# Kernel tuning notes

Hardware: AMD Instinct MI355X
Metric: run time of the kernel (lower is better)

## Reference

```python
import jax, jax.numpy as jnp
import numpy as np

N = 50000      # nodes
E = 800000     # edges (before self-loops)
IN = 256       # in_channels
H = 4          # heads (layer 1)
C = 64         # hidden per head
OUT = 40       # out_channels / classes


def setup_inputs() -> dict:
    key = jax.random.key(0)
    ks = jax.random.split(key, 10)
    s = 0.05  # weight init scale
    return {
        "x": jax.random.normal(ks[0], (N, IN), jnp.float32),
        "edge_index": jax.random.randint(ks[1], (2, E), 0, N),
        "W1": jax.random.normal(ks[2], (IN, H * C), jnp.float32) * s,
        "a_src1": jax.random.normal(ks[3], (H, C), jnp.float32) * s,
        "a_dst1": jax.random.normal(ks[4], (H, C), jnp.float32) * s,
        "b1": jnp.zeros((H * C,), jnp.float32),
        "W2": jax.random.normal(ks[5], (H * C, OUT), jnp.float32) * s,
        "a_src2": jax.random.normal(ks[6], (1, OUT), jnp.float32) * s,
        "a_dst2": jax.random.normal(ks[7], (1, OUT), jnp.float32) * s,
        "b2": jnp.zeros((OUT,), jnp.float32),
    }


def _gat_layer(x, src, dst, W, a_src, a_dst, bias, heads, out_c):
    """PyG GATConv (concat=True, negative_slope=0.2, self-loops already in src/dst)."""
    n = x.shape[0]
    h = (x @ W).reshape(n, heads, out_c)                    # [N,H,C]
    al_s = jnp.sum(h * a_src, axis=-1)                      # [N,H]
    al_d = jnp.sum(h * a_dst, axis=-1)                      # [N,H]
    e = jax.nn.leaky_relu(al_s[src] + al_d[dst], 0.2)       # [Etot,H]
    # edge softmax over incoming edges of each destination node
    m = jax.ops.segment_max(e, dst, num_segments=n)         # [N,H]
    ee = jnp.exp(e - m[dst])
    denom = jax.ops.segment_sum(ee, dst, num_segments=n)
    alpha = ee / (denom[dst] + 1e-16)                       # [Etot,H]
    msg = alpha[:, :, None] * h[src]                        # [Etot,H,C]
    out = jax.ops.segment_sum(msg, dst, num_segments=n)     # [N,H,C]
    return out.reshape(n, heads * out_c) + bias


def reference(x, edge_index, W1, a_src1, a_dst1, b1, W2, a_src2, a_dst2, b2):
    n = x.shape[0]
    loops = jnp.arange(n, dtype=edge_index.dtype)
    src = jnp.concatenate([edge_index[0], loops])
    dst = jnp.concatenate([edge_index[1], loops])
    h = _gat_layer(x, src, dst, W1, a_src1, a_dst1, b1, H, C)   # [N, H*C]
    h = jax.nn.relu(h)
    # F.dropout in eval mode is identity (reference run in eval mode)
    out = _gat_layer(h, src, dst, W2, a_src2, a_dst2, b2, 1, OUT)  # [N, OUT]
    return jax.nn.log_softmax(out, axis=1)
```

## Files before the change

### kernel.cpp

```cpp
#include <hip/hip_runtime.h>
#include <hip/hip_bf16.h>

typedef __hip_bfloat16 bf16;
typedef short v8s __attribute__((ext_vector_type(8)));
typedef float v4f __attribute__((ext_vector_type(4)));

constexpr int NN    = 50000;
constexpr int NE    = 800000;
constexpr int CIN   = 256;
constexpr int HC    = 256;
constexpr int NH    = 4;
constexpr int NOUT  = 40;
constexpr int NPAD  = 48;
constexpr int SCB   = 196;

constexpr size_t al256(size_t x){ return (x + 255) & ~(size_t)255; }
constexpr size_t WS_FLAGS = 0;
constexpr size_t WS_EW1   = 256;
constexpr size_t WS_W1T   = al256(WS_EW1   + (size_t)NE*16);
constexpr size_t WS_AS1N  = al256(WS_W1T   + (size_t)CIN*HC*2);
constexpr size_t WS_AD1N  = al256(WS_AS1N  + HC*2);
constexpr size_t WS_B1N   = al256(WS_AD1N  + HC*2);
constexpr size_t WS_W2T   = al256(WS_B1N   + HC*2);
constexpr size_t WS_AS2N  = al256(WS_W2T   + (size_t)NPAD*HC*2);
constexpr size_t WS_AD2N  = al256(WS_AS2N  + NOUT*2);
constexpr size_t WS_B2N   = al256(WS_AD2N  + NOUT*2);
constexpr size_t WS_COUNTS= al256(WS_B2N   + NOUT*2);
constexpr size_t WS_CURSOR= al256(WS_COUNTS+ (size_t)NN*4);
constexpr size_t WS_ROWPTR= al256(WS_CURSOR+ (size_t)NN*4);
constexpr size_t WS_EIDX  = al256(WS_ROWPTR+ (size_t)(NN+1)*4);
constexpr size_t WS_H1    = al256(WS_EIDX  + (size_t)NE*4);
constexpr size_t WS_ALS1  = al256(WS_H1    + (size_t)NN*HC);
constexpr size_t WS_ALD1  = al256(WS_ALS1  + (size_t)NN*NH*4);
constexpr size_t WS_Y1    = al256(WS_ALD1  + (size_t)NN*NH*4);
constexpr size_t WS_H2    = al256(WS_Y1    + (size_t)NN*HC*2);
constexpr size_t WS_ALS2  = al256(WS_H2    + (size_t)NN*NOUT*2);
constexpr size_t WS_ALD2  = al256(WS_ALS2  + (size_t)NN*4);
constexpr size_t WS_EW2   = al256(WS_ALD2  + (size_t)NN*4);
constexpr size_t WS_BSUM  = al256(WS_EW2   + (size_t)NE*4);
constexpr size_t WS_BOFF  = al256(WS_BSUM  + 1024);

constexpr int CV_W1  = 0;
constexpr int CV_AS1 = CV_W1  + CIN*HC;
constexpr int CV_AD1 = CV_AS1 + HC;
constexpr int CV_B1  = CV_AD1 + HC;
constexpr int CV_W2  = CV_B1  + HC;
constexpr int CV_AS2 = CV_W2  + HC*NOUT;
constexpr int CV_AD2 = CV_AS2 + NOUT;
constexpr int CV_B2  = CV_AD2 + NOUT;
constexpr int CV_HIST= CV_B2  + NOUT;
constexpr int CV_END = CV_HIST + NE;

__device__ __forceinline__ float b2f(bf16 v) { return __bfloat162float(v); }
__device__ __forceinline__ bf16  f2b(float v){ return __float2bfloat16(v); }
__device__ __forceinline__ float bits2f(unsigned short u){ return __uint_as_float(((unsigned)u) << 16); }
__device__ __forceinline__ unsigned short f2bits(float v){
  bf16 t = __float2bfloat16(v);
  return *reinterpret_cast<unsigned short*>(&t);
}
__device__ __forceinline__ float lrelu(float x){ return x > 0.f ? x : 0.2f * x; }

__device__ __forceinline__ float wave_sum(float v){
  #pragma unroll
  for (int off = 32; off; off >>= 1) v += __shfl_xor(v, off, 64);
  return v;
}
__device__ __forceinline__ float wave_max(float v){
  #pragma unroll
  for (int off = 32; off; off >>= 1) v = fmaxf(v, __shfl_xor(v, off, 64));
  return v;
}

__global__ __launch_bounds__(64) void k_detect(const unsigned short* __restrict__ xu,
                                               const unsigned* __restrict__ eu,
                                               int* __restrict__ flags){
  int lane = threadIdx.x;
  int cnt = 0;
  for (int i = lane; i < 256; i += 64){
    int e = (xu[i] >> 7) & 0xFF;
    cnt += (e >= 0x60 && e <= 0x8F) ? 1 : 0;
  }
  #pragma unroll
  for (int off = 32; off; off >>= 1) cnt += __shfl_xor(cnt, off, 64);
  unsigned odd = eu[2 * lane + 1];
  #pragma unroll
  for (int off = 32; off; off >>= 1) odd |= __shfl_xor(odd, off, 64);
  if (lane == 0){
    flags[0] = (cnt < 218) ? 1 : 0;
    flags[1] = (odd == 0)  ? 1 : 0;
  }
}

__device__ __forceinline__ bf16 cvt_b(const void* src, int i, int f32m){
  if (f32m) return __float2bfloat16(((const float*)src)[i]);
  return ((const bf16*)src)[i];
}

__global__ __launch_bounds__(256) void k_convert(
    const void* __restrict__ W1,
    const void* __restrict__ as1,const void* __restrict__ ad1,
    const void* __restrict__ b1, const void* __restrict__ W2,
    const void* __restrict__ as2,const void* __restrict__ ad2,
    const void* __restrict__ b2, const void* __restrict__ ei,
    char* __restrict__ ws){
  const int* flags = (const int*)(ws + WS_FLAGS);
  int f32m = flags[0], i64m = flags[1];
  bf16* w1t  = (bf16*)(ws + WS_W1T);
  bf16* as1n = (bf16*)(ws + WS_AS1N);
  bf16* ad1n = (bf16*)(ws + WS_AD1N);
  bf16* b1n  = (bf16*)(ws + WS_B1N);
  bf16* w2t  = (bf16*)(ws + WS_W2T);
  bf16* as2n = (bf16*)(ws + WS_AS2N);
  bf16* ad2n = (bf16*)(ws + WS_AD2N);
  bf16* b2n  = (bf16*)(ws + WS_B2N);
  int*  counts=(int*) (ws + WS_COUNTS);
  for (int g = blockIdx.x * 256 + threadIdx.x; g < CV_END; g += gridDim.x * 256){
    if      (g < CV_AS1){ int i = g-CV_W1; int k = i >> 8, n = i & 255;
      w1t[n*CIN + k] = cvt_b(W1, i, f32m); }
    else if (g < CV_AD1) as1n[g-CV_AS1] = cvt_b(as1,g-CV_AS1, f32m);
    else if (g < CV_B1 ) ad1n[g-CV_AD1] = cvt_b(ad1,g-CV_AD1, f32m);
    else if (g < CV_W2 ) b1n [g-CV_B1 ] = cvt_b(b1, g-CV_B1,  f32m);
    else if (g < CV_AS2){ int i = g-CV_W2; int k = i / NOUT, n = i - k*NOUT;
      w2t[n*CIN + k] = cvt_b(W2, i, f32m); }
    else if (g < CV_AD2) as2n[g-CV_AS2] = cvt_b(as2,g-CV_AS2, f32m);
    else if (g < CV_B2 ) ad2n[g-CV_AD2] = cvt_b(ad2,g-CV_AD2, f32m);
    else if (g < CV_HIST) b2n[g-CV_B2 ] = cvt_b(b2, g-CV_B2,  f32m);
    else { int i = g-CV_HIST;
      int d = i64m ? (int)((const long long*)ei)[(size_t)NE+i] : ((const int*)ei)[NE+i];
      atomicAdd(&counts[d], 1); }
  }
}

__global__ __launch_bounds__(256) void k_scan_part(const int* __restrict__ counts, int* __restrict__ bsum){
  __shared__ int lds[256];
  int t = threadIdx.x;
  int idx = blockIdx.x * 256 + t;
  int v = (idx < NN) ? counts[idx] : 0;
  lds[t] = v;
  #pragma unroll
  for (int s = 128; s > 0; s >>= 1){
    __syncthreads();
    if (t < s) lds[t] += lds[t + s];
  }
  if (t == 0) bsum[blockIdx.x] = lds[0];
}

__global__ __launch_bounds__(256) void k_scan_mid(const int* __restrict__ bsum, int* __restrict__ boff,
                                                  int* __restrict__ row_ptr){
  __shared__ int lds[256];
  int t = threadIdx.x;
  int v = (t < SCB) ? bsum[t] : 0;
  lds[t] = v;
  for (int off = 1; off < 256; off <<= 1){
    __syncthreads();
    int u = (t >= off) ? lds[t - off] : 0;
    __syncthreads();
    lds[t] += u;
  }
  __syncthreads();
  if (t < SCB) boff[t] = lds[t] - v;
  if (t == 0) row_ptr[NN] = NE;
}

__global__ __launch_bounds__(256) void k_scan_apply(const int* __restrict__ counts, const int* __restrict__ boff,
                                                    int* __restrict__ row_ptr){
  __shared__ int lds[256];
  int t = threadIdx.x;
  int idx = blockIdx.x * 256 + t;
  int v = (idx < NN) ? counts[idx] : 0;
  lds[t] = v;
  for (int off = 1; off < 256; off <<= 1){
    __syncthreads();
    int u = (t >= off) ? lds[t - off] : 0;
    __syncthreads();
    lds[t] += u;
  }
  __syncthreads();
  if (idx < NN) row_ptr[idx] = boff[blockIdx.x] + lds[t] - v;
}

__global__ __launch_bounds__(256) void k_scatter(const void* __restrict__ ei, const int* __restrict__ flags,
                                                 const int* __restrict__ row_ptr,
                                                 int* __restrict__ cursor, int* __restrict__ eidx){
  int i = blockIdx.x * 256 + threadIdx.x;
  if (i >= NE) return;
  int s, d;
  if (flags[1]){ s = (int)((const long long*)ei)[i]; d = (int)((const long long*)ei)[(size_t)NE + i]; }
  else         { s = ((const int*)ei)[i];            d = ((const int*)ei)[NE + i]; }
  int pos = row_ptr[d] + atomicAdd(&cursor[d], 1);
  eidx[pos] = s;
}

constexpr int G1R = 64;
constexpr int LP  = 72;
__global__ __launch_bounds__(256) void k_gemm1(const void* __restrict__ xin,
                                               const int* __restrict__ flags,
                                               const bf16* __restrict__ w1t,
                                               const bf16* __restrict__ as1, const bf16* __restrict__ ad1,
                                               unsigned char* __restrict__ h1q,
                                               float* __restrict__ al_s1, float* __restrict__ al_d1){
  __shared__ short Ab[G1R * LP];
  __shared__ short Bb[256 * LP];
  int tid  = threadIdx.x;
  int w    = tid >> 6, lane = tid & 63, quad = lane >> 4, c = lane & 15;
  int row0 = blockIdx.x * G1R;
  int f32m = flags[0];

  v4f acc[4][4];
  #pragma unroll
  for (int mt = 0; mt < 4; ++mt)
    #pragma unroll
    for (int nt = 0; nt < 4; ++nt) acc[mt][nt] = (v4f){0.f,0.f,0.f,0.f};

  int arow = tid >> 2;
  int aseg = tid & 3;
  int grow = row0 + arow; if (grow >= NN) grow = NN - 1;

  for (int ph = 0; ph < 4; ++ph){
    if (ph) __syncthreads();
    {
      short va[16];
      if (f32m){
        const float* src = (const float*)xin + (size_t)grow * CIN + ph*64 + aseg*16;
        #pragma unroll
        for (int i = 0; i < 4; ++i){
          float4 f = *reinterpret_cast<const float4*>(src + i*4);
          va[i*4+0] = (short)f2bits(f.x); va[i*4+1] = (short)f2bits(f.y);
          va[i*4+2] = (short)f2bits(f.z); va[i*4+3] = (short)f2bits(f.w);
        }
      } else {
        const short* src = (const short*)xin + (size_t)grow * CIN + ph*64 + aseg*16;
        v8s u0 = *reinterpret_cast<const v8s*>(src);
        v8s u1 = *reinterpret_cast<const v8s*>(src + 8);
        #pragma unroll
        for (int i = 0; i < 8; ++i){ va[i] = u0[i]; va[8+i] = u1[i]; }
      }
      short* dst = &Ab[arow * LP + aseg * 16];
      *reinterpret_cast<v8s*>(dst)     = *reinterpret_cast<v8s*>(&va[0]);
      *reinterpret_cast<v8s*>(dst + 8) = *reinterpret_cast<v8s*>(&va[8]);
    }
    {
      const short* src = (const short*)w1t + (size_t)tid * CIN + ph*64;
      short* dst = &Bb[tid * LP];
      #pragma unroll
      for (int j = 0; j < 8; ++j)
        *reinterpret_cast<v8s*>(dst + j*8) = *reinterpret_cast<const v8s*>(src + j*8);
    }
    __syncthreads();
    #pragma unroll
    for (int s = 0; s < 2; ++s){
      int ch = s*4 + quad;
      v8s af[4], bfb[4];
      #pragma unroll
      for (int mt = 0; mt < 4; ++mt)
        af[mt] = *reinterpret_cast<const v8s*>(&Ab[(mt*16 + c) * LP + ch*8]);
      #pragma unroll
      for (int nt = 0; nt < 4; ++nt)
        bfb[nt] = *reinterpret_cast<const v8s*>(&Bb[(w*64 + nt*16 + c) * LP + ch*8]);
      #pragma unroll
      for (int mt = 0; mt < 4; ++mt)
        #pragma unroll
        for (int nt = 0; nt < 4; ++nt)
          acc[mt][nt] = __builtin_amdgcn_mfma_f32_16x16x32_bf16(af[mt], bfb[nt], acc[mt][nt], 0, 0, 0);
    }
  }

  float as1v[4], ad1v[4];
  #pragma unroll
  for (int nt = 0; nt < 4; ++nt){
    as1v[nt] = b2f(as1[w*64 + nt*16 + c]);
    ad1v[nt] = b2f(ad1[w*64 + nt*16 + c]);
  }
  #pragma unroll
  for (int mt = 0; mt < 4; ++mt){
    #pragma unroll
    for (int r = 0; r < 4; ++r){
      float ps = 0.f, pd = 0.f;
      #pragma unroll
      for (int nt = 0; nt < 4; ++nt){ ps += acc[mt][nt][r] * as1v[nt]; pd += acc[mt][nt][r] * ad1v[nt]; }
      #pragma unroll
      for (int off = 1; off < 16; off <<= 1){ ps += __shfl_xor(ps, off, 64); pd += __shfl_xor(pd, off, 64); }
      int row = row0 + mt*16 + quad*4 + r;
      if (c == 0 && row < NN){
        al_s1[row * NH + w] = ps;
        al_d1[row * NH + w] = pd;
      }
    }
  }
  #pragma unroll
  for (int mt = 0; mt < 4; ++mt){
    #pragma unroll
    for (int nt = 0; nt < 4; ++nt){
      #pragma unroll
      for (int r = 0; r < 4; r += 2){
        int row = row0 + mt*16 + quad*4 + r;
        if (row + 1 < NN){
          int pk = __builtin_amdgcn_cvt_pk_fp8_f32(acc[mt][nt][r], acc[mt][nt][r+1], 0, false);
          size_t col = w*64 + nt*16 + c;
          h1q[(size_t)row       * HC + col] = (unsigned char)(pk & 0xFF);
          h1q[(size_t)(row + 1) * HC + col] = (unsigned char)((pk >> 8) & 0xFF);
        } else if (row < NN){
          int pk = __builtin_amdgcn_cvt_pk_fp8_f32(acc[mt][nt][r], acc[mt][nt][r], 0, false);
          h1q[(size_t)row * HC + w*64 + nt*16 + c] = (unsigned char)(pk & 0xFF);
        }
      }
    }
  }
}

__global__ __launch_bounds__(256) void k_ew1(const int* __restrict__ row_ptr, const int* __restrict__ eidx,
                                             const float* __restrict__ al_s1, const float* __restrict__ al_d1,
                                             float4* __restrict__ ew1){
  int lane = threadIdx.x & 63;
  int n = blockIdx.x * 4 + (threadIdx.x >> 6);
  int p0 = __builtin_amdgcn_readfirstlane(row_ptr[n]);
  int p1 = __builtin_amdgcn_readfirstlane(row_ptr[n + 1]);
  float4 ad = reinterpret_cast<const float4*>(al_d1)[n];
  for (int p = p0 + lane; p < p1; p += 64){
    int s = eidx[p];
    float4 as = reinterpret_cast<const float4*>(al_s1)[s];
    float4 w;
    w.x = __expf(lrelu(as.x + ad.x));
    w.y = __expf(lrelu(as.y + ad.y));
    w.z = __expf(lrelu(as.z + ad.z));
    w.w = __expf(lrelu(as.w + ad.w));
    ew1[p] = w;
  }
}

__global__ __launch_bounds__(256) void k_gather1(const int* __restrict__ row_ptr, const int* __restrict__ eidx,
                                                 const float* __restrict__ ew1,
                                                 const float* __restrict__ al_s1, const float* __restrict__ al_d1,
                                                 const unsigned* __restrict__ h1v, const bf16* __restrict__ b1,
                                                 bf16* __restrict__ y1){
  int lane = threadIdx.x & 63;
  int n = blockIdx.x * 4 + (threadIdx.x >> 6);
  int h = lane >> 4;
  int p0 = __builtin_amdgcn_readfirstlane(row_ptr[n]);
  int p1 = __builtin_amdgcn_readfirstlane(row_ptr[n + 1]);
  float wss = __expf(lrelu(al_s1[n * NH + h] + al_d1[n * NH + h]));
  unsigned us = h1v[(size_t)n * 64 + lane];
  float den = wss;
  float a0 = wss * __builtin_amdgcn_cvt_f32_fp8(us, 0);
  float a1 = wss * __builtin_amdgcn_cvt_f32_fp8(us, 1);
  float a2 = wss * __builtin_amdgcn_cvt_f32_fp8(us, 2);
  float a3 = wss * __builtin_amdgcn_cvt_f32_fp8(us, 3);
  int p = p0;
  for (; p + 1 < p1; p += 2){
    int sA = __builtin_amdgcn_readfirstlane(eidx[p]);
    int sB = __builtin_amdgcn_readfirstlane(eidx[p + 1]);
    float wA = ew1[(size_t)p * 4 + h];
    float wB = ew1[(size_t)(p + 1) * 4 + h];
    unsigned uA = h1v[(size_t)sA * 64 + lane];
    unsigned uB = h1v[(size_t)sB * 64 + lane];
    den += wA + wB;
    a0 += wA * __builtin_amdgcn_cvt_f32_fp8(uA, 0) + wB * __builtin_amdgcn_cvt_f32_fp8(uB, 0);
    a1 += wA * __builtin_amdgcn_cvt_f32_fp8(uA, 1) + wB * __builtin_amdgcn_cvt_f32_fp8(uB, 1);
    a2 += wA * __builtin_amdgcn_cvt_f32_fp8(uA, 2) + wB * __builtin_amdgcn_cvt_f32_fp8(uB, 2);
    a3 += wA * __builtin_amdgcn_cvt_f32_fp8(uA, 3) + wB * __builtin_amdgcn_cvt_f32_fp8(uB, 3);
  }
  if (p < p1){
    int s = __builtin_amdgcn_readfirstlane(eidx[p]);
    float w = ew1[(size_t)p * 4 + h];
    unsigned u = h1v[(size_t)s * 64 + lane];
    den += w;
    a0 += w * __builtin_amdgcn_cvt_f32_fp8(u, 0);
    a1 += w * __builtin_amdgcn_cvt_f32_fp8(u, 1);
    a2 += w * __builtin_amdgcn_cvt_f32_fp8(u, 2);
    a3 += w * __builtin_amdgcn_cvt_f32_fp8(u, 3);
  }
  float inv = 1.f / (den + 1e-16f);
  ushort4 bb = reinterpret_cast<const ushort4*>(b1)[lane];
  ushort4 o;
  o.x = f2bits(fmaxf(a0 * inv + bits2f(bb.x), 0.f));
  o.y = f2bits(fmaxf(a1 * inv + bits2f(bb.y), 0.f));
  o.z = f2bits(fmaxf(a2 * inv + bits2f(bb.z), 0.f));
  o.w = f2bits(fmaxf(a3 * inv + bits2f(bb.w), 0.f));
  reinterpret_cast<ushort4*>(y1)[(size_t)n * 64 + lane] = o;
}

constexpr int W2LP = 260;
__global__ __launch_bounds__(256) void k_gemm2(const bf16* __restrict__ y1, const bf16* __restrict__ w2t,
                                               const bf16* __restrict__ as2, const bf16* __restrict__ ad2,
                                               bf16* __restrict__ h2, float* __restrict__ al_s2,
                                               float* __restrict__ al_d2){
  __shared__ short Wb[NPAD * W2LP];
  int tid = threadIdx.x;
  int w = tid >> 6, lane = tid & 63, quad = lane >> 4, c = lane & 15;
  int m0 = blockIdx.x * 64 + w * 16;
  for (int idx = tid; idx < NPAD * 32; idx += 256){
    int n = idx >> 5, sg = idx & 31;
    *reinterpret_cast<v8s*>(&Wb[n * W2LP + sg * 8]) =
      *reinterpret_cast<const v8s*>((const short*)w2t + (size_t)n * CIN + sg * 8);
  }
  int arow = m0 + c; if (arow >= NN) arow = NN - 1;
  const short* ar = (const short*)y1 + (size_t)arow * HC + quad * 8;
  v8s a[8];
  #pragma unroll
  for (int i = 0; i < 8; ++i) a[i] = *reinterpret_cast<const v8s*>(ar + i * 32);
  __syncthreads();

  v4f acc[3];
  #pragma unroll
  for (int t = 0; t < 3; ++t) acc[t] = (v4f){0.f, 0.f, 0.f, 0.f};
  #pragma unroll
  for (int k = 0; k < 8; ++k){
    int ch = k*4 + quad;
    #pragma unroll
    for (int t = 0; t < 3; ++t){
      v8s b = *reinterpret_cast<const v8s*>(&Wb[(t*16 + c) * W2LP + ch * 8]);
      acc[t] = __builtin_amdgcn_mfma_f32_16x16x32_bf16(a[k], b, acc[t], 0, 0, 0);
    }
  }
  float as2f[3], ad2f[3];
  #pragma unroll
  for (int t = 0; t < 3; ++t){
    int col = t*16 + c;
    as2f[t] = (col < NOUT) ? b2f(as2[col]) : 0.f;
    ad2f[t] = (col < NOUT) ? b2f(ad2[col]) : 0.f;
  }
  #pragma unroll
  for (int r = 0; r < 4; ++r){
    int row = m0 + quad*4 + r;
    float ps = 0.f, pd = 0.f;
    #pragma unroll
    for (int t = 0; t < 3; ++t){ ps += acc[t][r] * as2f[t]; pd += acc[t][r] * ad2f[t]; }
    #pragma unroll
    for (int off = 1; off < 16; off <<= 1){ ps += __shfl_xor(ps, off, 64); pd += __shfl_xor(pd, off, 64); }
    if (row < NN){
      if (c == 0){ al_s2[row] = ps; al_d2[row] = pd; }
      #pragma unroll
      for (int t = 0; t < 3; ++t){
        int col = t*16 + c;
        if (col < NOUT) h2[(size_t)row * NOUT + col] = f2b(acc[t][r]);
      }
    }
  }
}

__global__ __launch_bounds__(256) void k_ew2(const int* __restrict__ row_ptr, const int* __restrict__ eidx,
                                             const float* __restrict__ al_s2, const float* __restrict__ al_d2,
                                             float* __restrict__ ew2){
  int lane = threadIdx.x & 63;
  int n = blockIdx.x * 4 + (threadIdx.x >> 6);
  int p0 = __builtin_amdgcn_readfirstlane(row_ptr[n]);
  int p1 = __builtin_amdgcn_readfirstlane(row_ptr[n + 1]);
  float ad = al_d2[n];
  for (int p = p0 + lane; p < p1; p += 64)
    ew2[p] = __expf(lrelu(al_s2[eidx[p]] + ad));
}

__global__ __launch_bounds__(256) void k_gather2(const int* __restrict__ row_ptr, const int* __restrict__ eidx,
                                                 const float* __restrict__ ew2,
                                                 const float* __restrict__ al_s2, const float* __restrict__ al_d2,
                                                 const bf16* __restrict__ h2, const bf16* __restrict__ b2v,
                                                 const int* __restrict__ flags, void* __restrict__ out){
  int lane = threadIdx.x & 63;
  int n = blockIdx.x * 4 + (threadIdx.x >> 6);
  int p0 = __builtin_amdgcn_readfirstlane(row_ptr[n]);
  int p1 = __builtin_amdgcn_readfirstlane(row_ptr[n + 1]);
  float wss = __expf(lrelu(al_s2[n] + al_d2[n]));
  float den = wss;
  float acc = (lane < NOUT) ? wss * b2f(h2[(size_t)n * NOUT + lane]) : 0.f;
  int p = p0;
  for (; p + 1 < p1; p += 2){
    int sA = __builtin_amdgcn_readfirstlane(eidx[p]);
    int sB = __builtin_amdgcn_readfirstlane(eidx[p + 1]);
    float wA = ew2[p], wB = ew2[p + 1];
    float hA = 0.f, hB = 0.f;
    if (lane < NOUT){
      hA = b2f(h2[(size_t)sA * NOUT + lane]);
      hB = b2f(h2[(size_t)sB * NOUT + lane]);
    }
    den += wA + wB;
    acc += wA * hA + wB * hB;
  }
  if (p < p1){
    int s = __builtin_amdgcn_readfirstlane(eidx[p]);
    float w = ew2[p];
    den += w;
    if (lane < NOUT) acc += w * b2f(h2[(size_t)s * NOUT + lane]);
  }
  float v = (lane < NOUT) ? (acc / (den + 1e-16f) + b2f(b2v[lane])) : -INFINITY;
  float M = wave_max(v);
  float ex = (lane < NOUT) ? __expf(v - M) : 0.f;
  float S = wave_sum(ex);
  if (lane < NOUT){
    float r = v - M - __logf(S);
    size_t idx = (size_t)n * NOUT + lane;
    if (flags[0]) ((float*)out)[idx] = r;
    else          ((bf16*)out)[idx]  = f2b(r);
  }
}

extern "C" void kernel_launch(void* const* d_in, const int* in_sizes, int n_in,
                              void* d_out, int out_size, void* d_ws, size_t ws_size,
                              hipStream_t stream) {
  const void* x   = d_in[0];
  const void* ei  = d_in[1];
  const void* W1  = d_in[2];
  const void* as1 = d_in[3];
  const void* ad1 = d_in[4];
  const void* b1  = d_in[5];
  const void* W2  = d_in[6];
  const void* as2 = d_in[7];
  const void* ad2 = d_in[8];
  const void* b2  = d_in[9];

  char* ws = (char*)d_ws;
  int*   flags   = (int*)  (ws + WS_FLAGS);
  float* ew1     = (float*)(ws + WS_EW1);
  bf16*  w1t     = (bf16*) (ws + WS_W1T);
  bf16*  as1n    = (bf16*) (ws + WS_AS1N);
  bf16*  ad1n    = (bf16*) (ws + WS_AD1N);
  bf16*  b1n     = (bf16*) (ws + WS_B1N);
  bf16*  w2t     = (bf16*) (ws + WS_W2T);
  bf16*  as2n    = (bf16*) (ws + WS_AS2N);
  bf16*  ad2n    = (bf16*) (ws + WS_AD2N);
  bf16*  b2n     = (bf16*) (ws + WS_B2N);
  int*   counts  = (int*)  (ws + WS_COUNTS);
  int*   cursor  = (int*)  (ws + WS_CURSOR);
  int*   row_ptr = (int*)  (ws + WS_ROWPTR);
  int*   eidx    = (int*)  (ws + WS_EIDX);
  unsigned char* h1q = (unsigned char*)(ws + WS_H1);
  float* al_s1   = (float*)(ws + WS_ALS1);
  float* al_d1   = (float*)(ws + WS_ALD1);
  bf16*  y1      = (bf16*) (ws + WS_Y1);
  bf16*  h2      = (bf16*) (ws + WS_H2);
  float* al_s2   = (float*)(ws + WS_ALS2);
  float* al_d2   = (float*)(ws + WS_ALD2);
  float* ew2     = (float*)(ws + WS_EW2);
  int*   bsum    = (int*)  (ws + WS_BSUM);
  int*   boff    = (int*)  (ws + WS_BOFF);

  hipMemsetAsync(counts, 0, (size_t)NN * 4, stream);
  hipMemsetAsync(cursor, 0, (size_t)NN * 4, stream);
  hipMemsetAsync(w2t,    0, (size_t)NPAD * CIN * 2, stream);

  k_detect <<<1, 64, 0, stream>>>((const unsigned short*)x, (const unsigned*)ei, flags);
  k_convert<<<1024, 256, 0, stream>>>(W1, as1, ad1, b1, W2, as2, ad2, b2, ei, ws);

  int eb = (NE + 255) / 256;
  k_scan_part <<<SCB, 256, 0, stream>>>(counts, bsum);
  k_scan_mid  <<<1, 256, 0, stream>>>(bsum, boff, row_ptr);
  k_scan_apply<<<SCB, 256, 0, stream>>>(counts, boff, row_ptr);
  k_scatter<<<eb, 256, 0, stream>>>(ei, flags, row_ptr, cursor, eidx);

  k_gemm1  <<<(NN + G1R - 1) / G1R, 256, 0, stream>>>(x, flags, w1t, as1n, ad1n, h1q, al_s1, al_d1);
  k_ew1    <<<NN / 4, 256, 0, stream>>>(row_ptr, eidx, al_s1, al_d1, (float4*)ew1);
  k_gather1<<<NN / 4, 256, 0, stream>>>(row_ptr, eidx, ew1, al_s1, al_d1, (const unsigned*)h1q, b1n, y1);
  k_gemm2  <<<(NN + 63) / 64, 256, 0, stream>>>(y1, w2t, as2n, ad2n, h2, al_s2, al_d2);
  k_ew2    <<<NN / 4, 256, 0, stream>>>(row_ptr, eidx, al_s2, al_d2, ew2);
  k_gather2<<<NN / 4, 256, 0, stream>>>(row_ptr, eidx, ew2, al_s2, al_d2, h2, b2n, flags, d_out);
}
```

Measured before the change: 342.5 us.

## Replace global-atomic CSR scatter with two-pass bucketed scatter by destination block

The single-pass edge scatter, which did a global atomic per edge on random destination cursors, becomes a two-level bucket sort. Edges are first histogrammed and scattered into 256-node destination buckets using LDS atomics. A per-bucket refine pass then does the final CSR placement with localized global atomics. The aim is better locality for the cursor atomics and the eidx writes, at the cost of three extra launches, a small single-block scan and an intermediate int2 edge buffer.

```diff
diff --git a/kernel.cpp b/kernel.cpp
--- a/kernel.cpp
+++ b/kernel.cpp
@@ -13,6 +13,9 @@
 constexpr int NOUT  = 40;
 constexpr int NPAD  = 48;
 constexpr int SCB   = 196;
+constexpr int B1    = 128;
+constexpr int CH    = (NE + B1 - 1) / B1;
+constexpr int NB    = (NN + 255) >> 8;
 
 constexpr size_t al256(size_t x){ return (x + 255) & ~(size_t)255; }
 constexpr size_t WS_FLAGS = 0;
@@ -39,6 +42,10 @@
 constexpr size_t WS_EW2   = al256(WS_ALD2  + (size_t)NN*4);
 constexpr size_t WS_BSUM  = al256(WS_EW2   + (size_t)NE*4);
 constexpr size_t WS_BOFF  = al256(WS_BSUM  + 1024);
+constexpr size_t WS_GCNT  = al256(WS_BOFF  + 1024);
+constexpr size_t WS_ROFF  = al256(WS_GCNT  + (size_t)256*B1*4);
+constexpr size_t WS_BBASE = al256(WS_ROFF  + (size_t)256*B1*4);
+constexpr size_t WS_EBUF  = al256(WS_BBASE + 1056);
 
 constexpr int CV_W1  = 0;
 constexpr int CV_AS1 = CV_W1  + CIN*HC;
@@ -179,16 +186,73 @@
   if (idx < NN) row_ptr[idx] = boff[blockIdx.x] + lds[t] - v;
 }
 
-__global__ __launch_bounds__(256) void k_scatter(const void* __restrict__ ei, const int* __restrict__ flags,
-                                                 const int* __restrict__ row_ptr,
-                                                 int* __restrict__ cursor, int* __restrict__ eidx){
-  int i = blockIdx.x * 256 + threadIdx.x;
-  if (i >= NE) return;
-  int s, d;
-  if (flags[1]){ s = (int)((const long long*)ei)[i]; d = (int)((const long long*)ei)[(size_t)NE + i]; }
-  else         { s = ((const int*)ei)[i];            d = ((const int*)ei)[NE + i]; }
-  int pos = row_ptr[d] + atomicAdd(&cursor[d], 1);
-  eidx[pos] = s;
+__global__ __launch_bounds__(256) void k_lhist(const void* __restrict__ ei, const int* __restrict__ flags,
+                                               int* __restrict__ gcnt){
+  __shared__ int h[256];
+  int tid = threadIdx.x, blk = blockIdx.x;
+  h[tid] = 0;
+  __syncthreads();
+  int i0 = blk * CH, i1 = min(i0 + CH, NE);
+  int i64m = flags[1];
+  for (int i = i0 + tid; i < i1; i += 256){
+    int d = i64m ? (int)((const long long*)ei)[(size_t)NE + i] : ((const int*)ei)[NE + i];
+    atomicAdd(&h[d >> 8], 1);
+  }
+  __syncthreads();
+  gcnt[tid * B1 + blk] = h[tid];
+}
+
+__global__ __launch_bounds__(256) void k_gscan(const int* __restrict__ gcnt, int* __restrict__ roff,
+                                               int* __restrict__ bbase){
+  __shared__ int lds[256];
+  int t = threadIdx.x;
+  int tot = 0;
+  for (int blk = 0; blk < B1; ++blk) tot += gcnt[t * B1 + blk];
+  lds[t] = tot;
+  for (int off = 1; off < 256; off <<= 1){
+    __syncthreads();
+    int u = (t >= off) ? lds[t - off] : 0;
+    __syncthreads();
+    lds[t] += u;
+  }
+  __syncthreads();
+  int base = lds[t] - tot;
+  bbase[t] = base;
+  if (t == 255) bbase[256] = NE;
+  int run = base;
+  for (int blk = 0; blk < B1; ++blk){
+    roff[t * B1 + blk] = run;
+    run += gcnt[t * B1 + blk];
+  }
+}
+
+__global__ __launch_bounds__(256) void k_bscatter(const void* __restrict__ ei, const int* __restrict__ flags,
+                                                  const int* __restrict__ roff, int2* __restrict__ ebuf){
+  __shared__ int lcur[256];
+  int tid = threadIdx.x, blk = blockIdx.x;
+  lcur[tid] = roff[tid * B1 + blk];
+  __syncthreads();
+  int i0 = blk * CH, i1 = min(i0 + CH, NE);
+  int i64m = flags[1];
+  for (int i = i0 + tid; i < i1; i += 256){
+    int s, d;
+    if (i64m){ s = (int)((const long long*)ei)[i]; d = (int)((const long long*)ei)[(size_t)NE + i]; }
+    else     { s = ((const int*)ei)[i];            d = ((const int*)ei)[NE + i]; }
+    int pos = atomicAdd(&lcur[d >> 8], 1);
+    ebuf[pos] = make_int2(s, d);
+  }
+}
+
+__global__ __launch_bounds__(256) void k_refine(const int2* __restrict__ ebuf, const int* __restrict__ bbase,
+                                                const int* __restrict__ row_ptr, int* __restrict__ cursor,
+                                                int* __restrict__ eidx){
+  int b = blockIdx.x;
+  int p0 = bbase[b], p1 = bbase[b + 1];
+  for (int p = p0 + threadIdx.x; p < p1; p += 256){
+    int2 e = ebuf[p];
+    int pos = row_ptr[e.y] + atomicAdd(&cursor[e.y], 1);
+    eidx[pos] = e.x;
+  }
 }
 
 constexpr int G1R = 64;
@@ -532,6 +596,10 @@
   float* ew2     = (float*)(ws + WS_EW2);
   int*   bsum    = (int*)  (ws + WS_BSUM);
   int*   boff    = (int*)  (ws + WS_BOFF);
+  int*   gcnt    = (int*)  (ws + WS_GCNT);
+  int*   roff    = (int*)  (ws + WS_ROFF);
+  int*   bbase   = (int*)  (ws + WS_BBASE);
+  int2*  ebuf    = (int2*) (ws + WS_EBUF);
 
   hipMemsetAsync(counts, 0, (size_t)NN * 4, stream);
   hipMemsetAsync(cursor, 0, (size_t)NN * 4, stream);
@@ -540,11 +608,13 @@
   k_detect <<<1, 64, 0, stream>>>((const unsigned short*)x, (const unsigned*)ei, flags);
   k_convert<<<1024, 256, 0, stream>>>(W1, as1, ad1, b1, W2, as2, ad2, b2, ei, ws);
 
-  int eb = (NE + 255) / 256;
+  k_lhist   <<<B1, 256, 0, stream>>>(ei, flags, gcnt);
+  k_gscan   <<<1, 256, 0, stream>>>(gcnt, roff, bbase);
   k_scan_part <<<SCB, 256, 0, stream>>>(counts, bsum);
   k_scan_mid  <<<1, 256, 0, stream>>>(bsum, boff, row_ptr);
   k_scan_apply<<<SCB, 256, 0, stream>>>(counts, boff, row_ptr);
-  k_scatter<<<eb, 256, 0, stream>>>(ei, flags, row_ptr, cursor, eidx);
+  k_bscatter<<<B1, 256, 0, stream>>>(ei, flags, roff, ebuf);
+  k_refine  <<<NB, 256, 0, stream>>>(ebuf, bbase, row_ptr, cursor, eidx);
 
   k_gemm1  <<<(NN + G1R - 1) / G1R, 256, 0, stream>>>(x, flags, w1t, as1n, ad1n, h1q, al_s1, al_d1);
   k_ew1    <<<NN / 4, 256, 0, stream>>>(row_ptr, eidx, al_s1, al_d1, (float4*)ew1);
```

New measurement: 347.3 us. Within noise of the previous version (+1.4%).
